# Performance work log

Measured on AMD Instinct MI355X. Metric: run time of the kernel, lower is better.

Reference implementation:

```python
import jax, jax.numpy as jnp
import numpy as np

EPS_DISC = 1e-9  # matches mamba_discretization denominator epsilon


def setup_inputs() -> dict:
    key = jax.random.key(0)
    ks = jax.random.split(key, 12)
    L, D, N, W = 2048, 1024, 16, 3
    s = 0.02  # small init scale to keep softplus/exp well-behaved
    u_seq = jax.random.normal(ks[0], (L, D), jnp.float32)
    # A_log = log(-A) with A = randn*0.1 - 1.0  -> log of a value near 1
    A_log = jnp.log(jnp.clip(1.0 - 0.1 * jax.random.normal(ks[1], (N,), jnp.float32), 0.5, 1.5))
    dt_w = jax.random.normal(ks[2], (D, D), jnp.float32) * s
    dt_b = jax.random.normal(ks[3], (D,), jnp.float32) * s
    B_w = jax.random.normal(ks[4], (N, D), jnp.float32) * s
    B_b = jax.random.normal(ks[5], (N,), jnp.float32) * s
    C_w = jax.random.normal(ks[6], (N, D), jnp.float32) * s
    C_b = jax.random.normal(ks[7], (N,), jnp.float32) * s
    D_w = jnp.ones((D,), jnp.float32)
    scale = jnp.ones((), jnp.float32)
    init_w = jax.random.normal(ks[8], (D * N, D * W), jnp.float32) * s
    init_b = jax.random.normal(ks[9], (D * N,), jnp.float32) * s
    return {"u_seq": u_seq, "A_log": A_log, "dt_w": dt_w, "dt_b": dt_b,
            "B_w": B_w, "B_b": B_b, "C_w": C_w, "C_b": C_b,
            "D_w": D_w, "scale": scale, "init_w": init_w, "init_b": init_b}


def reference(u_seq, A_log, dt_w, dt_b, B_w, B_b, C_w, C_b, D_w, scale, init_w, init_b):
    L, D = u_seq.shape
    N = A_log.shape[0]
    init_window = init_w.shape[1] // D
    # Initial state h0 = init_estimator(u[:W].flatten()).view(D, N)
    u_prefix = u_seq[:init_window].reshape(-1)
    h0 = (u_prefix @ init_w.T + init_b).reshape(D, N)
    # Input-dependent SSM parameters (all L timesteps at once)
    dt = jax.nn.softplus(u_seq @ dt_w.T + dt_b)           # [L, D]
    B = u_seq @ B_w.T + B_b                               # [L, N]
    C = u_seq @ C_w.T + C_b                               # [L, N]
    A = -jnp.exp(A_log)                                   # [N]
    dtA = dt[:, :, None] * A                              # [L, D, N]
    dA = jnp.exp(dtA)                                     # [L, D, N]
    dB = jnp.expm1(dtA) / (dtA + EPS_DISC) * B[:, None, :]  # ZOH discretization
    Bu = dB * u_seq[:, :, None]                           # [L, D, N]

    # Sequential selective-scan recurrence: h_t = dA_t * h_{t-1} + Bu_t
    def step(h, inp):
        dA_t, Bu_t = inp
        h = dA_t * h + Bu_t
        return h, h

    _, h_hist = jax.lax.scan(step, h0, (dA, Bu))          # [L, D, N]
    y_raw = jnp.einsum('ln,ldn->ld', C, h_hist) + D_w * u_seq
    return jax.nn.softplus(y_raw) * jnp.maximum(scale, 0.5)
```

## Files before the change

kernel.cpp:

```cpp
#include <hip/hip_runtime.h>
#include <hip/hip_bf16.h>

typedef __attribute__((ext_vector_type(8))) short short8v;
typedef __attribute__((ext_vector_type(4))) float f32x4;

#define L_SEQ 2048
#define D_DIM 1024
#define N_DIM 16
#define T_CHUNK 32
#define NCHUNK (L_SEQ / T_CHUNK)
#define EPS_DISC 1e-9f

__device__ __forceinline__ float softplusf(float x) {
    return (x > 15.f) ? x : __logf(1.f + __expf(x));
}

__device__ __forceinline__ unsigned short f2bf(float f) {
    unsigned int u = __float_as_uint(f);
    u += 0x7FFFu + ((u >> 16) & 1u);
    return (unsigned short)(u >> 16);
}
__device__ __forceinline__ unsigned int pack2(float a, float b) {
    return (unsigned int)f2bf(a) | ((unsigned int)f2bf(b) << 16);
}

__global__ __launch_bounds__(256) void k_params(const float* __restrict__ u,
                                                const float* __restrict__ dt_w,
                                                const float* __restrict__ dt_b,
                                                const float* __restrict__ B_w,
                                                const float* __restrict__ B_b,
                                                const float* __restrict__ C_w,
                                                const float* __restrict__ C_b,
                                                const float* __restrict__ init_w,
                                                const float* __restrict__ init_b,
                                                float* __restrict__ dt,
                                                float* __restrict__ Bm,
                                                float* __restrict__ Cm,
                                                float* __restrict__ h0) {
    __shared__ unsigned int As[64 * 16];
    __shared__ unsigned int Bs[128 * 16];
    const int tile = blockIdx.x;
    const int t = threadIdx.x;

    if (tile < 256) {
        const int bm = tile & 31;
        const int bn = tile >> 5;
        const int lane = t & 63;
        const int wn   = t >> 6;
        const int lrow = lane & 15, lq = lane >> 4;

        const int arow = t >> 2, aq = t & 3;
        const int brow = t >> 1, bhalf = t & 1;

        const float* uptr = u + (bm * 64 + arow) * 1024 + aq * 8;
        const float* wptr = dt_w + (bn * 128 + brow) * 1024 + bhalf * 16;

        f32x4 acc[4][2];
#pragma unroll
        for (int mi = 0; mi < 4; ++mi)
#pragma unroll
            for (int ni = 0; ni < 2; ++ni) acc[mi][ni] = (f32x4){0.f, 0.f, 0.f, 0.f};

        for (int k0 = 0; k0 < 1024; k0 += 32) {
            __syncthreads();
            {
                const float4* p = (const float4*)(uptr + k0);
                float4 a0 = p[0], a1 = p[1];
                uint4 ca = make_uint4(pack2(a0.x, a0.y), pack2(a0.z, a0.w),
                                      pack2(a1.x, a1.y), pack2(a1.z, a1.w));
                const int akb = aq ^ ((arow >> 1) & 3);
                *(uint4*)&As[arow * 16 + akb * 4] = ca;

                const float4* q = (const float4*)(wptr + k0);
                float4 b0 = q[0], b1 = q[1], b2 = q[2], b3 = q[3];
                uint4 d0 = make_uint4(pack2(b0.x, b0.y), pack2(b0.z, b0.w),
                                      pack2(b1.x, b1.y), pack2(b1.z, b1.w));
                uint4 d1 = make_uint4(pack2(b2.x, b2.y), pack2(b2.z, b2.w),
                                      pack2(b3.x, b3.y), pack2(b3.z, b3.w));
                const int bswz = (brow >> 1) & 3;
                const int kb0 = (bhalf * 2) ^ bswz, kb1 = (bhalf * 2 + 1) ^ bswz;
                *(uint4*)&Bs[brow * 16 + kb0 * 4] = d0;
                *(uint4*)&Bs[brow * 16 + kb1 * 4] = d1;
            }
            __syncthreads();
            short8v af[4], bf[2];
#pragma unroll
            for (int mi = 0; mi < 4; ++mi) {
                const int ar = mi * 16 + lrow;
                const int kb = lq ^ ((ar >> 1) & 3);
                af[mi] = *(const short8v*)&As[ar * 16 + kb * 4];
            }
#pragma unroll
            for (int ni = 0; ni < 2; ++ni) {
                const int br = wn * 32 + ni * 16 + lrow;
                const int kb = lq ^ ((br >> 1) & 3);
                bf[ni] = *(const short8v*)&Bs[br * 16 + kb * 4];
            }
#pragma unroll
            for (int mi = 0; mi < 4; ++mi)
#pragma unroll
                for (int ni = 0; ni < 2; ++ni)
                    acc[mi][ni] = __builtin_amdgcn_mfma_f32_16x16x32_bf16(af[mi], bf[ni], acc[mi][ni], 0, 0, 0);
        }

#pragma unroll
        for (int mi = 0; mi < 4; ++mi)
#pragma unroll
            for (int ni = 0; ni < 2; ++ni) {
                const int cg = bn * 128 + wn * 32 + ni * 16 + lrow;
                const float bv = dt_b[cg];
#pragma unroll
                for (int j = 0; j < 4; ++j) {
                    const int rg = bm * 64 + mi * 16 + lq * 4 + j;
                    dt[rg * 1024 + cg] = softplusf(acc[mi][ni][j] + bv);
                }
            }
    } else if (tile < 512) {
        const int tid = (tile - 256) * 256 + t;
        const int l = tid >> 5;
        const int col = tid & 31;
        const float* wrow = (col < 16) ? (B_w + col * 1024) : (C_w + (col - 16) * 1024);
        const float4* w4 = (const float4*)wrow;
        const float4* u4 = (const float4*)(u + l * 1024);
        float acc = 0.f;
#pragma unroll 8
        for (int j = 0; j < 256; ++j) {
            float4 a = u4[j], bb = w4[j];
            acc += a.x * bb.x + a.y * bb.y + a.z * bb.z + a.w * bb.w;
        }
        if (col < 16) Bm[l * 16 + col] = acc + B_b[col];
        else          Cm[l * 16 + (col - 16)] = acc + C_b[col - 16];
    } else {
        const int lane = t & 63;
        const int row  = (tile - 512) * 4 + (t >> 6);
        const float4* w4 = (const float4*)(init_w + row * 3072);
        const float4* u4 = (const float4*)u;
        float acc = 0.f;
#pragma unroll
        for (int s = 0; s < 12; ++s) {
            float4 a = w4[s * 64 + lane];
            float4 bb = u4[s * 64 + lane];
            acc += a.x * bb.x + a.y * bb.y + a.z * bb.z + a.w * bb.w;
        }
#pragma unroll
        for (int off = 32; off > 0; off >>= 1) acc += __shfl_down(acc, off);
        if (lane == 0) h0[row] = acc + init_b[row];
    }
}

__global__ __launch_bounds__(256) void k_p1(const float* __restrict__ dt,
                                            const float* __restrict__ Bm,
                                            const float* __restrict__ u,
                                            const float* __restrict__ A_log,
                                            float* __restrict__ ap,
                                            float* __restrict__ hl) {
    const int t    = threadIdx.x;
    const int c    = blockIdx.x >> 3;
    const int dblk = blockIdx.x & 7;
    const int dd   = t >> 1;
    const int nh   = t & 1;
    const int d    = dblk * 128 + dd;
    float An[8];
#pragma unroll
    for (int n = 0; n < 8; ++n) An[n] = -__expf(A_log[nh * 8 + n]);
    float h[8], p[8];
#pragma unroll
    for (int n = 0; n < 8; ++n) { h[n] = 0.f; p[n] = 1.f; }

    const int l0 = c * T_CHUNK;
    for (int i = 0; i < T_CHUNK; ++i) {
        const int l = l0 + i;
        const float dtld = dt[l * D_DIM + d];
        const float uld  = u[l * D_DIM + d];
        const float4 b0 = *(const float4*)&Bm[l * 16 + nh * 8];
        const float4 b1 = *(const float4*)&Bm[l * 16 + nh * 8 + 4];
        auto body = [&](int n, float bn) {
            const float x = dtld * An[n];
            const float e = __expf(x);
            const float coef = (e - 1.f) * __builtin_amdgcn_rcpf(x + EPS_DISC);
            const float bu = coef * bn * uld;
            p[n] *= e;
            h[n] = fmaf(e, h[n], bu);
        };
        body(0, b0.x); body(1, b0.y); body(2, b0.z); body(3, b0.w);
        body(4, b1.x); body(5, b1.y); body(6, b1.z); body(7, b1.w);
    }
    const int base = c * (D_DIM * N_DIM) + d * 16 + nh * 8;
    *(float4*)&ap[base + 0] = make_float4(p[0], p[1], p[2], p[3]);
    *(float4*)&ap[base + 4] = make_float4(p[4], p[5], p[6], p[7]);
    *(float4*)&hl[base + 0] = make_float4(h[0], h[1], h[2], h[3]);
    *(float4*)&hl[base + 4] = make_float4(h[4], h[5], h[6], h[7]);
}

__global__ __launch_bounds__(64) void k_p2(const float* __restrict__ h0,
                                           float* __restrict__ ap,
                                           const float* __restrict__ hl) {
    const int ch = blockIdx.x * 64 + threadIdx.x;
    float h = h0[ch];
#pragma unroll 8
    for (int c = 0; c < NCHUNK; ++c) {
        const int idx = c * (D_DIM * N_DIM) + ch;
        const float a = ap[idx];
        const float b = hl[idx];
        ap[idx] = h;
        h = fmaf(a, h, b);
    }
}

__global__ __launch_bounds__(256) void k_p3(const float* __restrict__ dt,
                                            const float* __restrict__ Bm,
                                            const float* __restrict__ Cm,
                                            const float* __restrict__ u,
                                            const float* __restrict__ A_log,
                                            const float* __restrict__ hstart,
                                            const float* __restrict__ D_w,
                                            const float* __restrict__ scale,
                                            float* __restrict__ out) {
    const int t    = threadIdx.x;
    const int c    = blockIdx.x >> 3;
    const int dblk = blockIdx.x & 7;
    const int dd   = t >> 1;
    const int nh   = t & 1;
    const int d    = dblk * 128 + dd;
    float An[8];
#pragma unroll
    for (int n = 0; n < 8; ++n) An[n] = -__expf(A_log[nh * 8 + n]);
    float h[8];
    const int base = c * (D_DIM * N_DIM) + d * 16 + nh * 8;
    {
        float4 h0v = *(const float4*)&hstart[base + 0];
        float4 h1v = *(const float4*)&hstart[base + 4];
        h[0] = h0v.x; h[1] = h0v.y; h[2] = h0v.z; h[3] = h0v.w;
        h[4] = h1v.x; h[5] = h1v.y; h[6] = h1v.z; h[7] = h1v.w;
    }
    const float scl = fmaxf(scale[0], 0.5f);
    const float dw = D_w[d];
    const int l0 = c * T_CHUNK;
    for (int i = 0; i < T_CHUNK; ++i) {
        const int l = l0 + i;
        const float dtld = dt[l * D_DIM + d];
        const float uld  = u[l * D_DIM + d];
        const float4 b0 = *(const float4*)&Bm[l * 16 + nh * 8];
        const float4 b1 = *(const float4*)&Bm[l * 16 + nh * 8 + 4];
        const float4 c0 = *(const float4*)&Cm[l * 16 + nh * 8];
        const float4 c1 = *(const float4*)&Cm[l * 16 + nh * 8 + 4];
        float y = 0.f;
        auto body = [&](int n, float bn, float cn) {
            const float x = dtld * An[n];
            const float e = __expf(x);
            const float coef = (e - 1.f) * __builtin_amdgcn_rcpf(x + EPS_DISC);
            const float bu = coef * bn * uld;
            h[n] = fmaf(e, h[n], bu);
            y = fmaf(cn, h[n], y);
        };
        body(0, b0.x, c0.x); body(1, b0.y, c0.y); body(2, b0.z, c0.z); body(3, b0.w, c0.w);
        body(4, b1.x, c1.x); body(5, b1.y, c1.y); body(6, b1.z, c1.z); body(7, b1.w, c1.w);
        y += __shfl_xor(y, 1);
        if (nh == 0) {
            const float yv = fmaf(dw, uld, y);
            out[l * D_DIM + d] = softplusf(yv) * scl;
        }
    }
}

extern "C" void kernel_launch(void* const* d_in, const int* in_sizes, int n_in,
                              void* d_out, int out_size, void* d_ws, size_t ws_size,
                              hipStream_t stream) {
    const float* u      = (const float*)d_in[0];
    const float* A_log  = (const float*)d_in[1];
    const float* dt_w   = (const float*)d_in[2];
    const float* dt_b   = (const float*)d_in[3];
    const float* B_w    = (const float*)d_in[4];
    const float* B_b    = (const float*)d_in[5];
    const float* C_w    = (const float*)d_in[6];
    const float* C_b    = (const float*)d_in[7];
    const float* D_w    = (const float*)d_in[8];
    const float* scale  = (const float*)d_in[9];
    const float* init_w = (const float*)d_in[10];
    const float* init_b = (const float*)d_in[11];
    float* out = (float*)d_out;

    float* ws = (float*)d_ws;
    float* dt = ws;
    float* Bm = dt + 2097152;
    float* Cm = Bm + 32768;
    float* h0 = Cm + 32768;
    float* ap = h0 + 16384;
    float* hl = ap + 1048576;

    hipLaunchKernelGGL(k_params, dim3(4608), dim3(256), 0, stream,
                       u, dt_w, dt_b, B_w, B_b, C_w, C_b, init_w, init_b,
                       dt, Bm, Cm, h0);
    hipLaunchKernelGGL(k_p1, dim3(512), dim3(256), 0, stream, dt, Bm, u, A_log, ap, hl);
    hipLaunchKernelGGL(k_p2, dim3(256), dim3(64), 0, stream, h0, ap, hl);
    hipLaunchKernelGGL(k_p3, dim3(512), dim3(256), 0, stream, dt, Bm, Cm, u, A_log, ap, D_w, scale, out);
}
```

Baseline: 119.2 us.

## Split parameter kernel into separate GEMM, B/C and init matvec kernels

Replaces the single heterogeneous k_params launch with three kernels: an MFMA GEMM for dt, a B/C projection kernel, and an init-state matvec. The matvec now has each block read 16 contiguous rows of the 200MB init_w with deep float4 prefetch and a shared-memory reduction, so that this bandwidth-bound load streams better. The B/C kernel keeps a row of u in registers and reduces across a wavefront with shuffles, replacing strided per-thread loops. The cost is two more kernel launches and serialized stages in place of one mixed grid.

```diff
diff --git a/kernel.cpp b/kernel.cpp
--- a/kernel.cpp
+++ b/kernel.cpp
@@ -23,128 +23,172 @@
 __device__ __forceinline__ unsigned int pack2(float a, float b) {
     return (unsigned int)f2bf(a) | ((unsigned int)f2bf(b) << 16);
 }
-
-__global__ __launch_bounds__(256) void k_params(const float* __restrict__ u,
-                                                const float* __restrict__ dt_w,
-                                                const float* __restrict__ dt_b,
-                                                const float* __restrict__ B_w,
-                                                const float* __restrict__ B_b,
-                                                const float* __restrict__ C_w,
-                                                const float* __restrict__ C_b,
-                                                const float* __restrict__ init_w,
-                                                const float* __restrict__ init_b,
-                                                float* __restrict__ dt,
-                                                float* __restrict__ Bm,
-                                                float* __restrict__ Cm,
-                                                float* __restrict__ h0) {
+__device__ __forceinline__ float dot4(float4 a, float4 b) {
+    return a.x * b.x + a.y * b.y + a.z * b.z + a.w * b.w;
+}
+
+__global__ __launch_bounds__(256) void k_mv(const float* __restrict__ u,
+                                            const float* __restrict__ init_w,
+                                            const float* __restrict__ init_b,
+                                            float* __restrict__ h0) {
+    __shared__ float sf[4096];
+    const int bid = blockIdx.x;
+    const int t = threadIdx.x;
+
+    const float4* u4 = (const float4*)u;
+    const float4 bb0 = u4[t];
+    const float4 bb1 = u4[t + 256];
+    const float4 bb2 = u4[t + 512];
+
+    const float4* w4 = (const float4*)init_w + (size_t)bid * 12288 + t;
+    float pr[16];
+
+    float4 a0[8], a1[8], a2[8];
+#pragma unroll
+    for (int q = 0; q < 8; ++q) {
+        a0[q] = w4[q * 768];
+        a1[q] = w4[q * 768 + 256];
+        a2[q] = w4[q * 768 + 512];
+    }
+#pragma unroll
+    for (int q = 0; q < 8; ++q)
+        pr[q] = dot4(a0[q], bb0) + dot4(a1[q], bb1) + dot4(a2[q], bb2);
+#pragma unroll
+    for (int q = 0; q < 8; ++q) {
+        a0[q] = w4[(q + 8) * 768];
+        a1[q] = w4[(q + 8) * 768 + 256];
+        a2[q] = w4[(q + 8) * 768 + 512];
+    }
+#pragma unroll
+    for (int q = 0; q < 8; ++q)
+        pr[q + 8] = dot4(a0[q], bb0) + dot4(a1[q], bb1) + dot4(a2[q], bb2);
+
+#pragma unroll
+    for (int q = 0; q < 16; ++q) sf[q * 256 + t] = pr[q];
+    __syncthreads();
+    const int r = t >> 4, i = t & 15;
+    float s = 0.f;
+#pragma unroll
+    for (int j = 0; j < 16; ++j) s += sf[r * 256 + i * 16 + j];
+#pragma unroll
+    for (int m = 8; m >= 1; m >>= 1) s += __shfl_xor(s, m, 16);
+    if (i == 0) {
+        const int row = bid * 16 + r;
+        h0[row] = s + init_b[row];
+    }
+}
+
+__global__ __launch_bounds__(256) void k_gemm(const float* __restrict__ u,
+                                              const float* __restrict__ dt_w,
+                                              const float* __restrict__ dt_b,
+                                              float* __restrict__ dt) {
     __shared__ unsigned int As[64 * 16];
     __shared__ unsigned int Bs[128 * 16];
     const int tile = blockIdx.x;
     const int t = threadIdx.x;
 
-    if (tile < 256) {
-        const int bm = tile & 31;
-        const int bn = tile >> 5;
-        const int lane = t & 63;
-        const int wn   = t >> 6;
-        const int lrow = lane & 15, lq = lane >> 4;
-
-        const int arow = t >> 2, aq = t & 3;
-        const int brow = t >> 1, bhalf = t & 1;
-
-        const float* uptr = u + (bm * 64 + arow) * 1024 + aq * 8;
-        const float* wptr = dt_w + (bn * 128 + brow) * 1024 + bhalf * 16;
-
-        f32x4 acc[4][2];
+    const int bm = tile & 31;
+    const int bn = tile >> 5;
+    const int lane = t & 63;
+    const int wn   = t >> 6;
+    const int lrow = lane & 15, lq = lane >> 4;
+
+    const int arow = t >> 2, aq = t & 3;
+    const int brow = t >> 1, bhalf = t & 1;
+
+    const float* uptr = u + (bm * 64 + arow) * 1024 + aq * 8;
+    const float* wptr = dt_w + (bn * 128 + brow) * 1024 + bhalf * 16;
+
+    f32x4 acc[4][2];
+#pragma unroll
+    for (int mi = 0; mi < 4; ++mi)
+#pragma unroll
+        for (int ni = 0; ni < 2; ++ni) acc[mi][ni] = (f32x4){0.f, 0.f, 0.f, 0.f};
+
+    for (int k0 = 0; k0 < 1024; k0 += 32) {
+        __syncthreads();
+        {
+            const float4* p = (const float4*)(uptr + k0);
+            float4 a0 = p[0], a1 = p[1];
+            uint4 ca = make_uint4(pack2(a0.x, a0.y), pack2(a0.z, a0.w),
+                                  pack2(a1.x, a1.y), pack2(a1.z, a1.w));
+            const int akb = aq ^ ((arow >> 1) & 3);
+            *(uint4*)&As[arow * 16 + akb * 4] = ca;
+
+            const float4* q = (const float4*)(wptr + k0);
+            float4 b0 = q[0], b1 = q[1], b2 = q[2], b3 = q[3];
+            uint4 d0 = make_uint4(pack2(b0.x, b0.y), pack2(b0.z, b0.w),
+                                  pack2(b1.x, b1.y), pack2(b1.z, b1.w));
+            uint4 d1 = make_uint4(pack2(b2.x, b2.y), pack2(b2.z, b2.w),
+                                  pack2(b3.x, b3.y), pack2(b3.z, b3.w));
+            const int bswz = (brow >> 1) & 3;
+            const int kb0 = (bhalf * 2) ^ bswz, kb1 = (bhalf * 2 + 1) ^ bswz;
+            *(uint4*)&Bs[brow * 16 + kb0 * 4] = d0;
+            *(uint4*)&Bs[brow * 16 + kb1 * 4] = d1;
+        }
+        __syncthreads();
+        short8v af[4], bf[2];
+#pragma unroll
+        for (int mi = 0; mi < 4; ++mi) {
+            const int ar = mi * 16 + lrow;
+            const int kb = lq ^ ((ar >> 1) & 3);
+            af[mi] = *(const short8v*)&As[ar * 16 + kb * 4];
+        }
+#pragma unroll
+        for (int ni = 0; ni < 2; ++ni) {
+            const int br = wn * 32 + ni * 16 + lrow;
+            const int kb = lq ^ ((br >> 1) & 3);
+            bf[ni] = *(const short8v*)&Bs[br * 16 + kb * 4];
+        }
 #pragma unroll
         for (int mi = 0; mi < 4; ++mi)
 #pragma unroll
-            for (int ni = 0; ni < 2; ++ni) acc[mi][ni] = (f32x4){0.f, 0.f, 0.f, 0.f};
-
-        for (int k0 = 0; k0 < 1024; k0 += 32) {
-            __syncthreads();
-            {
-                const float4* p = (const float4*)(uptr + k0);
-                float4 a0 = p[0], a1 = p[1];
-                uint4 ca = make_uint4(pack2(a0.x, a0.y), pack2(a0.z, a0.w),
-                                      pack2(a1.x, a1.y), pack2(a1.z, a1.w));
-                const int akb = aq ^ ((arow >> 1) & 3);
-                *(uint4*)&As[arow * 16 + akb * 4] = ca;
-
-                const float4* q = (const float4*)(wptr + k0);
-                float4 b0 = q[0], b1 = q[1], b2 = q[2], b3 = q[3];
-                uint4 d0 = make_uint4(pack2(b0.x, b0.y), pack2(b0.z, b0.w),
-                                      pack2(b1.x, b1.y), pack2(b1.z, b1.w));
-                uint4 d1 = make_uint4(pack2(b2.x, b2.y), pack2(b2.z, b2.w),
-                                      pack2(b3.x, b3.y), pack2(b3.z, b3.w));
-                const int bswz = (brow >> 1) & 3;
-                const int kb0 = (bhalf * 2) ^ bswz, kb1 = (bhalf * 2 + 1) ^ bswz;
-                *(uint4*)&Bs[brow * 16 + kb0 * 4] = d0;
-                *(uint4*)&Bs[brow * 16 + kb1 * 4] = d1;
+            for (int ni = 0; ni < 2; ++ni)
+                acc[mi][ni] = __builtin_amdgcn_mfma_f32_16x16x32_bf16(af[mi], bf[ni], acc[mi][ni], 0, 0, 0);
+    }
+
+#pragma unroll
+    for (int mi = 0; mi < 4; ++mi)
+#pragma unroll
+        for (int ni = 0; ni < 2; ++ni) {
+            const int cg = bn * 128 + wn * 32 + ni * 16 + lrow;
+            const float bv = dt_b[cg];
+#pragma unroll
+            for (int j = 0; j < 4; ++j) {
+                const int rg = bm * 64 + mi * 16 + lq * 4 + j;
+                dt[rg * 1024 + cg] = softplusf(acc[mi][ni][j] + bv);
             }
-            __syncthreads();
-            short8v af[4], bf[2];
-#pragma unroll
-            for (int mi = 0; mi < 4; ++mi) {
-                const int ar = mi * 16 + lrow;
-                const int kb = lq ^ ((ar >> 1) & 3);
-                af[mi] = *(const short8v*)&As[ar * 16 + kb * 4];
-            }
-#pragma unroll
-            for (int ni = 0; ni < 2; ++ni) {
-                const int br = wn * 32 + ni * 16 + lrow;
-                const int kb = lq ^ ((br >> 1) & 3);
-                bf[ni] = *(const short8v*)&Bs[br * 16 + kb * 4];
-            }
-#pragma unroll
-            for (int mi = 0; mi < 4; ++mi)
-#pragma unroll
-                for (int ni = 0; ni < 2; ++ni)
-                    acc[mi][ni] = __builtin_amdgcn_mfma_f32_16x16x32_bf16(af[mi], bf[ni], acc[mi][ni], 0, 0, 0);
-        }
-
-#pragma unroll
-        for (int mi = 0; mi < 4; ++mi)
-#pragma unroll
-            for (int ni = 0; ni < 2; ++ni) {
-                const int cg = bn * 128 + wn * 32 + ni * 16 + lrow;
-                const float bv = dt_b[cg];
-#pragma unroll
-                for (int j = 0; j < 4; ++j) {
-                    const int rg = bm * 64 + mi * 16 + lq * 4 + j;
-                    dt[rg * 1024 + cg] = softplusf(acc[mi][ni][j] + bv);
-                }
-            }
-    } else if (tile < 512) {
-        const int tid = (tile - 256) * 256 + t;
-        const int l = tid >> 5;
-        const int col = tid & 31;
-        const float* wrow = (col < 16) ? (B_w + col * 1024) : (C_w + (col - 16) * 1024);
-        const float4* w4 = (const float4*)wrow;
-        const float4* u4 = (const float4*)(u + l * 1024);
-        float acc = 0.f;
-#pragma unroll 8
-        for (int j = 0; j < 256; ++j) {
-            float4 a = u4[j], bb = w4[j];
-            acc += a.x * bb.x + a.y * bb.y + a.z * bb.z + a.w * bb.w;
-        }
-        if (col < 16) Bm[l * 16 + col] = acc + B_b[col];
-        else          Cm[l * 16 + (col - 16)] = acc + C_b[col - 16];
-    } else {
-        const int lane = t & 63;
-        const int row  = (tile - 512) * 4 + (t >> 6);
-        const float4* w4 = (const float4*)(init_w + row * 3072);
-        const float4* u4 = (const float4*)u;
-        float acc = 0.f;
-#pragma unroll
-        for (int s = 0; s < 12; ++s) {
-            float4 a = w4[s * 64 + lane];
-            float4 bb = u4[s * 64 + lane];
-            acc += a.x * bb.x + a.y * bb.y + a.z * bb.z + a.w * bb.w;
-        }
-#pragma unroll
-        for (int off = 32; off > 0; off >>= 1) acc += __shfl_down(acc, off);
-        if (lane == 0) h0[row] = acc + init_b[row];
+        }
+}
+
+__global__ __launch_bounds__(256) void k_bc(const float* __restrict__ u,
+                                            const float* __restrict__ B_w,
+                                            const float* __restrict__ B_b,
+                                            const float* __restrict__ C_w,
+                                            const float* __restrict__ C_b,
+                                            float* __restrict__ Bm,
+                                            float* __restrict__ Cm) {
+    const int t = threadIdx.x;
+    const int lane = t & 63;
+    const int l = blockIdx.x * 4 + (t >> 6);
+    const float4* u4 = (const float4*)(u + l * 1024);
+    float4 ur[4];
+#pragma unroll
+    for (int i = 0; i < 4; ++i) ur[i] = u4[i * 64 + lane];
+
+#pragma unroll 4
+    for (int c = 0; c < 32; ++c) {
+        const float4* wr = (const float4*)((c < 16) ? (B_w + c * 1024)
+                                                    : (C_w + (c - 16) * 1024));
+        float s = 0.f;
+#pragma unroll
+        for (int i = 0; i < 4; ++i) s += dot4(ur[i], wr[i * 64 + lane]);
+#pragma unroll
+        for (int off = 32; off > 0; off >>= 1) s += __shfl_down(s, off);
+        if (lane == 0) {
+            if (c < 16) Bm[l * 16 + c] = s + B_b[c];
+            else        Cm[l * 16 + (c - 16)] = s + C_b[c - 16];
+        }
     }
 }
 
@@ -288,10 +332,10 @@
     float* ap = h0 + 16384;
     float* hl = ap + 1048576;
 
-    hipLaunchKernelGGL(k_params, dim3(4608), dim3(256), 0, stream,
-                       u, dt_w, dt_b, B_w, B_b, C_w, C_b, init_w, init_b,
-                       dt, Bm, Cm, h0);
-    hipLaunchKernelGGL(k_p1, dim3(512), dim3(256), 0, stream, dt, Bm, u, A_log, ap, hl);
-    hipLaunchKernelGGL(k_p2, dim3(256), dim3(64), 0, stream, h0, ap, hl);
-    hipLaunchKernelGGL(k_p3, dim3(512), dim3(256), 0, stream, dt, Bm, Cm, u, A_log, ap, D_w, scale, out);
-}
+    hipLaunchKernelGGL(k_mv,   dim3(1024), dim3(256), 0, stream, u, init_w, init_b, h0);
+    hipLaunchKernelGGL(k_gemm, dim3(256),  dim3(256), 0, stream, u, dt_w, dt_b, dt);
+    hipLaunchKernelGGL(k_bc,   dim3(512),  dim3(256), 0, stream, u, B_w, B_b, C_w, C_b, Bm, Cm);
+    hipLaunchKernelGGL(k_p1,   dim3(512),  dim3(256), 0, stream, dt, Bm, u, A_log, ap, hl);
+    hipLaunchKernelGGL(k_p2,   dim3(256),  dim3(64),  0, stream, h0, ap, hl);
+    hipLaunchKernelGGL(k_p3,   dim3(512),  dim3(256), 0, stream, dt, Bm, Cm, u, A_log, ap, D_w, scale, out);
+}
```

Result: slower. 136.9 us (+14.9%).

## Rebalance k_params block mix and restructure init and B/C projections

Applied to the files above, without the earlier changes.

Grid shrinks from 4608 to 1536 blocks. Every third block runs a dt GEMM or B/C tile, and the other two compute 16 rows of the init_w GEMV each: four rows per wave, with nontemporal loads and the u prefix reused across rows. The B/C projection switches from one thread per output with a serial 1024-long dot product to wave-cooperative dot products with shuffle reductions, giving coalesced loads. The intent is to interleave the bandwidth-bound 200MB init_w stream with the compute-bound GEMM blocks, cut per-block overhead, and fix uncoalesced B/C access; more registers per thread may limit occupancy.

```diff
diff --git a/kernel.cpp b/kernel.cpp
--- a/kernel.cpp
+++ b/kernel.cpp
@@ -23,28 +23,73 @@
 __device__ __forceinline__ unsigned int pack2(float a, float b) {
     return (unsigned int)f2bf(a) | ((unsigned int)f2bf(b) << 16);
 }
-
-__global__ __launch_bounds__(256) void k_params(const float* __restrict__ u,
-                                                const float* __restrict__ dt_w,
-                                                const float* __restrict__ dt_b,
-                                                const float* __restrict__ B_w,
-                                                const float* __restrict__ B_b,
-                                                const float* __restrict__ C_w,
-                                                const float* __restrict__ C_b,
-                                                const float* __restrict__ init_w,
-                                                const float* __restrict__ init_b,
-                                                float* __restrict__ dt,
-                                                float* __restrict__ Bm,
-                                                float* __restrict__ Cm,
-                                                float* __restrict__ h0) {
-    __shared__ unsigned int As[64 * 16];
-    __shared__ unsigned int Bs[128 * 16];
-    const int tile = blockIdx.x;
+__device__ __forceinline__ float dot4(float4 a, float4 b) {
+    return a.x * b.x + a.y * b.y + a.z * b.z + a.w * b.w;
+}
+__device__ __forceinline__ float dot4v(f32x4 a, f32x4 b) {
+    return a.x * b.x + a.y * b.y + a.z * b.z + a.w * b.w;
+}
+
+__global__ __launch_bounds__(256, 4) void k_params(const float* __restrict__ u,
+                                                   const float* __restrict__ dt_w,
+                                                   const float* __restrict__ dt_b,
+                                                   const float* __restrict__ B_w,
+                                                   const float* __restrict__ B_b,
+                                                   const float* __restrict__ C_w,
+                                                   const float* __restrict__ C_b,
+                                                   const float* __restrict__ init_w,
+                                                   const float* __restrict__ init_b,
+                                                   float* __restrict__ dt,
+                                                   float* __restrict__ Bm,
+                                                   float* __restrict__ Cm,
+                                                   float* __restrict__ h0) {
+    __shared__ unsigned int smem[3072];
+    const int b = blockIdx.x;
     const int t = threadIdx.x;
-
-    if (tile < 256) {
-        const int bm = tile & 31;
-        const int bn = tile >> 5;
+    const int r3 = b % 3;
+
+    if (r3 != 2) {
+        const int m = 2 * (b / 3) + r3;
+        const int wv = t >> 6, lane = t & 63;
+        const int r0 = m * 16 + wv * 4;
+        const f32x4* u4 = (const f32x4*)u;
+        f32x4 uu[12];
+#pragma unroll
+        for (int i = 0; i < 12; ++i) uu[i] = u4[i * 64 + lane];
+        float rs[4];
+#pragma unroll
+        for (int j = 0; j < 4; ++j) {
+            const f32x4* w4 = (const f32x4*)init_w + (size_t)(r0 + j) * 768;
+            f32x4 wr[12];
+#pragma unroll
+            for (int i = 0; i < 12; ++i)
+                wr[i] = __builtin_nontemporal_load(&w4[i * 64 + lane]);
+            float s0 = 0.f, s1 = 0.f, s2 = 0.f;
+#pragma unroll
+            for (int i = 0; i < 4; ++i) {
+                s0 += dot4v(wr[i], uu[i]);
+                s1 += dot4v(wr[i + 4], uu[i + 4]);
+                s2 += dot4v(wr[i + 8], uu[i + 8]);
+            }
+            rs[j] = s0 + s1 + s2;
+        }
+#pragma unroll
+        for (int j = 0; j < 4; ++j)
+#pragma unroll
+            for (int mm = 32; mm >= 1; mm >>= 1) rs[j] += __shfl_xor(rs[j], mm);
+        if (lane == 0) {
+#pragma unroll
+            for (int j = 0; j < 4; ++j) h0[r0 + j] = rs[j] + init_b[r0 + j];
+        }
+        return;
+    }
+
+    const int s = b / 3;
+    if (s < 256) {
+        unsigned int* As = smem;
+        unsigned int* Bs = smem + 1024;
+        const int bm = s & 31;
+        const int bn = s >> 5;
         const int lane = t & 63;
         const int wn   = t >> 6;
         const int lrow = lane & 15, lq = lane >> 4;
@@ -115,36 +160,31 @@
                     dt[rg * 1024 + cg] = softplusf(acc[mi][ni][j] + bv);
                 }
             }
-    } else if (tile < 512) {
-        const int tid = (tile - 256) * 256 + t;
-        const int l = tid >> 5;
-        const int col = tid & 31;
-        const float* wrow = (col < 16) ? (B_w + col * 1024) : (C_w + (col - 16) * 1024);
-        const float4* w4 = (const float4*)wrow;
-        const float4* u4 = (const float4*)(u + l * 1024);
-        float acc = 0.f;
-#pragma unroll 8
-        for (int j = 0; j < 256; ++j) {
-            float4 a = u4[j], bb = w4[j];
-            acc += a.x * bb.x + a.y * bb.y + a.z * bb.z + a.w * bb.w;
-        }
-        if (col < 16) Bm[l * 16 + col] = acc + B_b[col];
-        else          Cm[l * 16 + (col - 16)] = acc + C_b[col - 16];
     } else {
-        const int lane = t & 63;
-        const int row  = (tile - 512) * 4 + (t >> 6);
-        const float4* w4 = (const float4*)(init_w + row * 3072);
-        const float4* u4 = (const float4*)u;
-        float acc = 0.f;
-#pragma unroll
-        for (int s = 0; s < 12; ++s) {
-            float4 a = w4[s * 64 + lane];
-            float4 bb = u4[s * 64 + lane];
-            acc += a.x * bb.x + a.y * bb.y + a.z * bb.z + a.w * bb.w;
-        }
-#pragma unroll
-        for (int off = 32; off > 0; off >>= 1) acc += __shfl_down(acc, off);
-        if (lane == 0) h0[row] = acc + init_b[row];
+        const int s2 = s - 256;
+        const int wv = t >> 6, lane = t & 63;
+#pragma unroll
+        for (int rep = 0; rep < 2; ++rep) {
+            const int l = s2 * 8 + wv * 2 + rep;
+            const float4* u4 = (const float4*)(u + l * 1024);
+            float4 ur[4];
+#pragma unroll
+            for (int i = 0; i < 4; ++i) ur[i] = u4[i * 64 + lane];
+#pragma unroll 4
+            for (int c = 0; c < 32; ++c) {
+                const float4* wr = (const float4*)((c < 16) ? (B_w + c * 1024)
+                                                            : (C_w + (c - 16) * 1024));
+                float sv = 0.f;
+#pragma unroll
+                for (int i = 0; i < 4; ++i) sv += dot4(ur[i], wr[i * 64 + lane]);
+#pragma unroll
+                for (int off = 32; off > 0; off >>= 1) sv += __shfl_down(sv, off);
+                if (lane == 0) {
+                    if (c < 16) Bm[l * 16 + c] = sv + B_b[c];
+                    else        Cm[l * 16 + (c - 16)] = sv + C_b[c - 16];
+                }
+            }
+        }
     }
 }
 
@@ -288,7 +328,7 @@
     float* ap = h0 + 16384;
     float* hl = ap + 1048576;
 
-    hipLaunchKernelGGL(k_params, dim3(4608), dim3(256), 0, stream,
+    hipLaunchKernelGGL(k_params, dim3(1536), dim3(256), 0, stream,
                        u, dt_w, dt_b, B_w, B_b, C_w, C_b, init_w, init_b,
                        dt, Bm, Cm, h0);
     hipLaunchKernelGGL(k_p1, dim3(512), dim3(256), 0, stream, dt, Bm, u, A_log, ap, hl);
```

Measured after the change: 119.2 us. No clear change (+0.0%).
